# Kernel tuning notes

Measured on AMD Instinct MI355X. Metric: run time of the kernel, lower is better.

The kernel has to match this reference:

```python
import jax, jax.numpy as jnp
import numpy as np

DIM = 2048          # SDR dimension
CTX = 512           # top-down context (grid code) dimension
B = 8192            # batch of independent samples
N_PV = DIM // 4     # 512 PV interneurons
N_SV = DIM // 8     # 256 SOM/VIP interneurons
ALPHA_POS = 1.0 / 10.0   # dt / tau_pos
ALPHA_NEG = 1.0 / 10.0   # dt / tau_neg


def setup_inputs() -> dict:
    key = jax.random.key(0)
    ks = jax.random.split(key, 14)
    sc = 1.0 / np.sqrt(DIM)
    sc_sv = 1.0 / np.sqrt(N_SV)
    xav = np.sqrt(6.0 / (CTX + DIM))  # xavier uniform bound for predictor
    u = lambda k, shp, s: jax.random.uniform(k, shp, dtype=jnp.float32) * s
    return {
        "x_batch": jax.random.uniform(ks[0], (B, DIM), dtype=jnp.float32),
        "context_batch": jax.random.normal(ks[1], (B, CTX), dtype=jnp.float32),
        "r_pos_batch": jax.random.uniform(ks[2], (B, DIM), dtype=jnp.float32),
        "r_neg_batch": jax.random.uniform(ks[3], (B, DIM), dtype=jnp.float32),
        "W_pred": jax.random.uniform(ks[4], (DIM, CTX), jnp.float32, -xav, xav),
        "b_pred": jnp.zeros((DIM,), jnp.float32),
        "W_pv1_ff": u(ks[5], (N_PV, DIM), sc),
        "W_pv2_td": u(ks[6], (N_PV, DIM), sc),
        "W_vip_td": u(ks[7], (N_SV, DIM), sc),
        "W_som_in": u(ks[8], (N_SV, DIM), sc),
        "W_vip_som": u(ks[9], (N_SV, N_SV), sc_sv),
        "W_inh_pe_pos": u(ks[10], (DIM, N_PV), sc),
        "W_inh_pe_neg": u(ks[11], (DIM, N_PV), sc),
        "W_som_dend": u(ks[12], (DIM, N_SV), sc),
    }


def reference(x_batch, context_batch, r_pos_batch, r_neg_batch,
              W_pred, b_pred, W_pv1_ff, W_pv2_td, W_vip_td, W_som_in,
              W_vip_som, W_inh_pe_pos, W_inh_pe_neg, W_som_dend):
    relu = jax.nn.relu
    # top-down prediction: (B, CTX) @ (CTX, DIM) -> (B, DIM)
    predicted = context_batch @ W_pred.T + b_pred
    # interneuron circuit (Nemati 2025)
    r_pv1 = relu(x_batch @ W_pv1_ff.T)                               # (B, N_PV)
    r_pv2 = relu(predicted @ W_pv2_td.T)                             # (B, N_PV)
    r_vip = relu(predicted @ W_vip_td.T)                             # (B, N_SV)
    r_som = relu(relu(x_batch @ W_som_in.T) - r_vip @ W_vip_som.T)   # (B, N_SV)
    # signed prediction errors with somatic/dendritic inhibition
    pe_pos = relu(x_batch - predicted - r_pv2 @ W_inh_pe_pos.T)
    pe_neg = relu(predicted - x_batch - r_pv1 @ W_inh_pe_neg.T - r_som @ W_som_dend.T)
    # low-pass temporal filter of PE states
    new_r_pos = (1.0 - ALPHA_POS) * r_pos_batch + ALPHA_POS * pe_pos
    new_r_neg = (1.0 - ALPHA_NEG) * r_neg_batch + ALPHA_NEG * pe_neg
    return (new_r_pos, new_r_neg)
```

## Files before the change

kernel.cpp:

```cpp
#include <hip/hip_runtime.h>
#include <hip/hip_bf16.h>
#include <stdint.h>
#include <stddef.h>

#define DIMV 2048
#define CTXV 512
#define BV   8192
#define NPV  512
#define NSV  256

typedef __attribute__((ext_vector_type(8))) __bf16 bf16x8;
typedef __attribute__((ext_vector_type(4))) float f32x4;

enum { EPI_BIAS = 0, EPI_RELU = 1, EPI_SUBR = 2, EPI_FILT = 3 };

__device__ __forceinline__ void gload_lds16(const void* g, void* l) {
    __builtin_amdgcn_global_load_lds(
        (const __attribute__((address_space(1))) unsigned int*)g,
        (__attribute__((address_space(3))) unsigned int*)l,
        16, 0, 0);
}

struct CvtArgs {
    const float* src[11];
    __bf16*      dst[11];
};

__global__ __launch_bounds__(256) void cvt_all(CvtArgs a) {
    constexpr int NSEG = 11;
    constexpr unsigned cum[NSEG + 1] = {
        0u, 2097152u, 2621440u, 2752512u, 2883584u, 3014656u,
        3080192u, 3145728u, 3153920u, 3284992u, 3416064u, 3481600u};
    const unsigned total = cum[NSEG];
    for (unsigned c = blockIdx.x * blockDim.x + threadIdx.x; c < total;
         c += gridDim.x * blockDim.x) {
        const float* sp = a.src[0];
        __bf16*      dp = a.dst[0];
        unsigned     base = 0;
#pragma unroll
        for (int t = 1; t < NSEG; ++t) {
            const bool g = (c >= cum[t]);
            sp   = g ? a.src[t] : sp;
            dp   = g ? a.dst[t] : dp;
            base = g ? cum[t] : base;
        }
        const unsigned off = (c - base) * 8u;
        f32x4 v0 = *(const f32x4*)(sp + off);
        f32x4 v1 = *(const f32x4*)(sp + off + 4);
        bf16x8 o;
#pragma unroll
        for (int e = 0; e < 4; ++e) { o[e] = (__bf16)v0[e]; o[e + 4] = (__bf16)v1[e]; }
        *(bf16x8*)(dp + off) = o;
    }
}

template <int EPI>
__global__ __launch_bounds__(256)
void pe_gemm(const __bf16* __restrict__ A, int ldA,
             const __bf16* __restrict__ A2, int ldA2, int ksA,
             const __bf16* __restrict__ W1, int ldW1,
             const __bf16* __restrict__ W1k2, int ldW1k2, int ksW,
             const __bf16* __restrict__ W2, int ldW2,
             int NB1, int N1cols, int N2cols, int K, int nbx,
             const float* __restrict__ bias,
             const __bf16* __restrict__ subp,
             const __bf16* __restrict__ predb, const float* __restrict__ xf,
             float sgn, const float* __restrict__ rold,
             void* __restrict__ out1, void* __restrict__ out2)
{
    __shared__ __align__(16) __bf16 ldsA[128 * 32];
    __shared__ __align__(16) __bf16 ldsB[128 * 32];
    char* ldsAb = (char*)ldsA;
    char* ldsBb = (char*)ldsB;

    const int nwg = gridDim.x;
    const int bid = blockIdx.x;
    const int wg  = (bid & 7) * (nwg >> 3) + (bid >> 3);
    const int bx  = wg % nbx;
    const int by  = wg / nbx;
    const int m0  = bx * 128;
    const int n0  = by * 128;

    const bool reg2   = (W2 != nullptr) && (n0 >= NB1);
    const __bf16* Wa  = reg2 ? W2 : W1;
    const __bf16* Wb  = W1k2;
    const int wlda    = reg2 ? ldW2 : ldW1;
    const int wldb    = ldW1k2;
    const int kswcur  = reg2 ? K : ksW;
    const int nrow0   = reg2 ? (n0 - NB1) : n0;

    const int tid  = threadIdx.x;
    const int wave = tid >> 6;
    const int lane = tid & 63;
    const int lhi  = lane >> 4;
    const int llo  = lane & 15;
    const int wr   = wave >> 1;
    const int wc   = wave & 1;

    const f32x4 fzero = {0.f, 0.f, 0.f, 0.f};
    f32x4 acc[4][4];
#pragma unroll
    for (int i = 0; i < 4; ++i)
#pragma unroll
        for (int j = 0; j < 4; ++j) acc[i][j] = fzero;

    const int rins = lane >> 2;
    const int ch   = lane & 3;

    for (int k0 = 0; k0 < K; k0 += 32) {
        __syncthreads();
#pragma unroll
        for (int half = 0; half < 2; ++half) {
            const int rt = wave * 32 + half * 16 + rins;
            const int kc = ch ^ ((rt >> 1) & 3);
            const int kg = k0 + kc * 8;
            {
                const __bf16* src = (kg < ksA)
                    ? A  + (size_t)(m0 + rt) * ldA  + kg
                    : A2 + (size_t)(m0 + rt) * ldA2 + (kg - ksA);
                gload_lds16(src, ldsAb + wave * 2048 + half * 1024);
            }
            {
                const __bf16* src = (kg < kswcur)
                    ? Wa + (size_t)(nrow0 + rt) * wlda + kg
                    : Wb + (size_t)(nrow0 + rt) * wldb + (kg - kswcur);
                gload_lds16(src, ldsBb + wave * 2048 + half * 1024);
            }
        }
        __syncthreads();

        bf16x8 af[4], bfr[4];
#pragma unroll
        for (int i = 0; i < 4; ++i) {
            const int r  = wr * 64 + i * 16 + llo;
            const int pc = lhi ^ ((r >> 1) & 3);
            af[i] = *(const bf16x8*)(ldsAb + r * 64 + pc * 16);
        }
#pragma unroll
        for (int j = 0; j < 4; ++j) {
            const int r  = wc * 64 + j * 16 + llo;
            const int pc = lhi ^ ((r >> 1) & 3);
            bfr[j] = *(const bf16x8*)(ldsBb + r * 64 + pc * 16);
        }
#pragma unroll
        for (int i = 0; i < 4; ++i)
#pragma unroll
            for (int j = 0; j < 4; ++j)
                acc[i][j] = __builtin_amdgcn_mfma_f32_16x16x32_bf16(af[i], bfr[j], acc[i][j], 0, 0, 0);
    }

#pragma unroll
    for (int i = 0; i < 4; ++i) {
#pragma unroll
        for (int j = 0; j < 4; ++j) {
            const int colg = n0 + wc * 64 + j * 16 + llo;
#pragma unroll
            for (int r = 0; r < 4; ++r) {
                const int rowg = m0 + wr * 64 + i * 16 + lhi * 4 + r;
                float v = acc[i][j][r];
                if constexpr (EPI == EPI_BIAS) {
                    v += bias[colg];
                    ((__bf16*)out1)[(size_t)rowg * N1cols + colg] = (__bf16)v;
                } else if constexpr (EPI == EPI_RELU) {
                    v = fmaxf(v, 0.f);
                    if (colg < NB1)
                        ((__bf16*)out1)[(size_t)rowg * N1cols + colg] = (__bf16)v;
                    else
                        ((__bf16*)out2)[(size_t)rowg * N2cols + (colg - NB1)] = (__bf16)v;
                } else if constexpr (EPI == EPI_SUBR) {
                    const size_t idx = (size_t)rowg * N1cols + colg;
                    v = fmaxf((float)subp[idx] - v, 0.f);
                    ((__bf16*)out1)[idx] = (__bf16)v;
                } else {
                    const size_t idx = (size_t)rowg * 2048 + colg;
                    const float d = sgn * (xf[idx] - (float)predb[idx]) - v;
                    ((float*)out1)[idx] = 0.9f * rold[idx] + 0.1f * fmaxf(d, 0.f);
                }
            }
        }
    }
}

extern "C" void kernel_launch(void* const* d_in, const int* in_sizes, int n_in,
                              void* d_out, int out_size, void* d_ws, size_t ws_size,
                              hipStream_t stream) {
    (void)in_sizes; (void)n_in; (void)out_size; (void)ws_size;

    const float* x       = (const float*)d_in[0];
    const float* ctx     = (const float*)d_in[1];
    const float* r_pos   = (const float*)d_in[2];
    const float* r_neg   = (const float*)d_in[3];
    const float* Wpred   = (const float*)d_in[4];
    const float* bpred   = (const float*)d_in[5];
    const float* Wpv1    = (const float*)d_in[6];
    const float* Wpv2    = (const float*)d_in[7];
    const float* Wvip    = (const float*)d_in[8];
    const float* Wsomin  = (const float*)d_in[9];
    const float* Wvipsom = (const float*)d_in[10];
    const float* Wpepos  = (const float*)d_in[11];
    const float* Wpeneg  = (const float*)d_in[12];
    const float* Wsomd   = (const float*)d_in[13];

    char* ws = (char*)d_ws;
    __bf16* x_bf      = (__bf16*)ws; ws += (size_t)BV * DIMV * 2;
    __bf16* ctx_bf    = (__bf16*)ws; ws += (size_t)BV * CTXV * 2;
    __bf16* pred_bf   = (__bf16*)ws; ws += (size_t)BV * DIMV * 2;
    __bf16* rpv1_bf   = (__bf16*)ws; ws += (size_t)BV * NPV * 2;
    __bf16* rpv2_bf   = (__bf16*)ws; ws += (size_t)BV * NPV * 2;
    __bf16* rvip_bf   = (__bf16*)ws; ws += (size_t)BV * NSV * 2;
    __bf16* ssom_bf   = (__bf16*)ws; ws += (size_t)BV * NSV * 2;
    __bf16* rsom_bf   = (__bf16*)ws; ws += (size_t)BV * NSV * 2;
    __bf16* Wpred_bf  = (__bf16*)ws; ws += (size_t)DIMV * CTXV * 2;
    __bf16* Wpv1_bf   = (__bf16*)ws; ws += (size_t)NPV * DIMV * 2;
    __bf16* Wpv2_bf   = (__bf16*)ws; ws += (size_t)NPV * DIMV * 2;
    __bf16* Wvip_bf   = (__bf16*)ws; ws += (size_t)NSV * DIMV * 2;
    __bf16* Wsomin_bf = (__bf16*)ws; ws += (size_t)NSV * DIMV * 2;
    __bf16* Wvipsom_bf= (__bf16*)ws; ws += (size_t)NSV * NSV * 2;
    __bf16* Wpepos_bf = (__bf16*)ws; ws += (size_t)DIMV * NPV * 2;
    __bf16* Wpeneg_bf = (__bf16*)ws; ws += (size_t)DIMV * NPV * 2;
    __bf16* Wsomd_bf  = (__bf16*)ws; ws += (size_t)DIMV * NSV * 2;

    float* out_pos = (float*)d_out;
    float* out_neg = out_pos + (size_t)BV * DIMV;

    CvtArgs ca;
    ca.src[0] = x;       ca.dst[0] = x_bf;
    ca.src[1] = ctx;     ca.dst[1] = ctx_bf;
    ca.src[2] = Wpred;   ca.dst[2] = Wpred_bf;
    ca.src[3] = Wpv1;    ca.dst[3] = Wpv1_bf;
    ca.src[4] = Wpv2;    ca.dst[4] = Wpv2_bf;
    ca.src[5] = Wvip;    ca.dst[5] = Wvip_bf;
    ca.src[6] = Wsomin;  ca.dst[6] = Wsomin_bf;
    ca.src[7] = Wvipsom; ca.dst[7] = Wvipsom_bf;
    ca.src[8] = Wpepos;  ca.dst[8] = Wpepos_bf;
    ca.src[9] = Wpeneg;  ca.dst[9] = Wpeneg_bf;
    ca.src[10] = Wsomd;  ca.dst[10] = Wsomd_bf;
    cvt_all<<<dim3(2048), dim3(256), 0, stream>>>(ca);

    dim3 blk(256);

    pe_gemm<EPI_BIAS><<<dim3(1024), blk, 0, stream>>>(
        ctx_bf, CTXV, nullptr, 0, CTXV,
        Wpred_bf, CTXV, nullptr, 0, CTXV, nullptr, 0,
        DIMV, DIMV, 0, CTXV, 64,
        bpred, nullptr, nullptr, nullptr, 0.f, nullptr, pred_bf, nullptr);

    pe_gemm<EPI_RELU><<<dim3(384), blk, 0, stream>>>(
        x_bf, DIMV, nullptr, 0, DIMV,
        Wpv1_bf, DIMV, nullptr, 0, DIMV, Wsomin_bf, DIMV,
        NPV, NPV, NSV, DIMV, 64,
        nullptr, nullptr, nullptr, nullptr, 0.f, nullptr, rpv1_bf, ssom_bf);

    pe_gemm<EPI_RELU><<<dim3(384), blk, 0, stream>>>(
        pred_bf, DIMV, nullptr, 0, DIMV,
        Wpv2_bf, DIMV, nullptr, 0, DIMV, Wvip_bf, DIMV,
        NPV, NPV, NSV, DIMV, 64,
        nullptr, nullptr, nullptr, nullptr, 0.f, nullptr, rpv2_bf, rvip_bf);

    pe_gemm<EPI_SUBR><<<dim3(128), blk, 0, stream>>>(
        rvip_bf, NSV, nullptr, 0, NSV,
        Wvipsom_bf, NSV, nullptr, 0, NSV, nullptr, 0,
        NSV, NSV, 0, NSV, 64,
        nullptr, ssom_bf, nullptr, nullptr, 0.f, nullptr, rsom_bf, nullptr);

    pe_gemm<EPI_FILT><<<dim3(1024), blk, 0, stream>>>(
        rpv2_bf, NPV, nullptr, 0, NPV,
        Wpepos_bf, NPV, nullptr, 0, NPV, nullptr, 0,
        DIMV, DIMV, 0, NPV, 64,
        nullptr, nullptr, pred_bf, x, 1.f, r_pos, out_pos, nullptr);

    pe_gemm<EPI_FILT><<<dim3(1024), blk, 0, stream>>>(
        rpv1_bf, NPV, rsom_bf, NSV, NPV,
        Wpeneg_bf, NPV, Wsomd_bf, NSV, NPV, nullptr, 0,
        DIMV, DIMV, 0, NPV + NSV, 64,
        nullptr, nullptr, pred_bf, x, -1.f, r_neg, out_neg, nullptr);
}
```

Before: 353.9 us.

## Double-buffer GEMM LDS, merge independent GEMM launches, vectorize epilogues

Replaces the templated GEMM with a descriptor-driven kernel that runs two independent GEMMs in one launch (pred + pv1/som, and the pos/neg filter GEMMs), cutting launches from six to four and filling the device better. The K loop becomes double-buffered, so global-to-LDS loads for the next step overlap MFMA on the current one, with one barrier per step. Swapping the MFMA operands makes each lane hold four consecutive columns, which allows vectorized bf16x4/f32x4 epilogue stores. The filter epilogue now reads the bf16 copy of x instead of fp32 x, trading a little precision for less traffic. LDS use doubles and the epilogue type becomes a runtime branch.

```diff
diff --git a/kernel.cpp b/kernel.cpp
--- a/kernel.cpp
+++ b/kernel.cpp
@@ -10,9 +10,8 @@
 #define NSV  256
 
 typedef __attribute__((ext_vector_type(8))) __bf16 bf16x8;
+typedef __attribute__((ext_vector_type(4))) __bf16 bf16x4;
 typedef __attribute__((ext_vector_type(4))) float f32x4;
-
-enum { EPI_BIAS = 0, EPI_RELU = 1, EPI_SUBR = 2, EPI_FILT = 3 };
 
 __device__ __forceinline__ void gload_lds16(const void* g, void* l) {
     __builtin_amdgcn_global_load_lds(
@@ -54,40 +53,41 @@
     }
 }
 
-template <int EPI>
+struct GemmDesc {
+    const __bf16* A0; const __bf16* A1; int ldA0, ldA1;
+    const __bf16* W1; const __bf16* W2; const __bf16* W1b; int ldW, ldWb;
+    int ksplit;
+    int NB1;
+    int N1cols, N2cols;
+    int K;
+    int epi;
+    const float* bias;
+    const __bf16* subp;
+    const __bf16* xbf; const __bf16* predb; const float* rold; float sgn;
+    void* out1; void* out2;
+};
+
 __global__ __launch_bounds__(256)
-void pe_gemm(const __bf16* __restrict__ A, int ldA,
-             const __bf16* __restrict__ A2, int ldA2, int ksA,
-             const __bf16* __restrict__ W1, int ldW1,
-             const __bf16* __restrict__ W1k2, int ldW1k2, int ksW,
-             const __bf16* __restrict__ W2, int ldW2,
-             int NB1, int N1cols, int N2cols, int K, int nbx,
-             const float* __restrict__ bias,
-             const __bf16* __restrict__ subp,
-             const __bf16* __restrict__ predb, const float* __restrict__ xf,
-             float sgn, const float* __restrict__ rold,
-             void* __restrict__ out1, void* __restrict__ out2)
+void pe_gemm2(GemmDesc dA_, GemmDesc dB_, int splitWg)
 {
-    __shared__ __align__(16) __bf16 ldsA[128 * 32];
-    __shared__ __align__(16) __bf16 ldsB[128 * 32];
-    char* ldsAb = (char*)ldsA;
-    char* ldsBb = (char*)ldsB;
+    __shared__ __align__(16) char ldsA[2][8192];
+    __shared__ __align__(16) char ldsB[2][8192];
 
     const int nwg = gridDim.x;
     const int bid = blockIdx.x;
-    const int wg  = (bid & 7) * (nwg >> 3) + (bid >> 3);
-    const int bx  = wg % nbx;
-    const int by  = wg / nbx;
-    const int m0  = bx * 128;
-    const int n0  = by * 128;
-
-    const bool reg2   = (W2 != nullptr) && (n0 >= NB1);
-    const __bf16* Wa  = reg2 ? W2 : W1;
-    const __bf16* Wb  = W1k2;
-    const int wlda    = reg2 ? ldW2 : ldW1;
-    const int wldb    = ldW1k2;
-    const int kswcur  = reg2 ? K : ksW;
-    const int nrow0   = reg2 ? (n0 - NB1) : n0;
+    int wg = (bid & 7) * (nwg >> 3) + (bid >> 3);
+    const bool second = (wg >= splitWg);
+    if (second) wg -= splitWg;
+    const GemmDesc d = second ? dB_ : dA_;
+
+    const int bx = wg & 63;
+    const int by = wg >> 6;
+    const int m0 = bx * 128;
+    const int n0 = by * 128;
+
+    const bool reg2   = (n0 >= d.NB1);
+    const __bf16* Wk0 = reg2 ? d.W2 : d.W1;
+    const int n0r     = reg2 ? (n0 - d.NB1) : n0;
 
     const int tid  = threadIdx.x;
     const int wave = tid >> 6;
@@ -96,6 +96,8 @@
     const int llo  = lane & 15;
     const int wr   = wave >> 1;
     const int wc   = wave & 1;
+    const int rins = lane >> 2;
+    const int ch   = lane & 3;
 
     const f32x4 fzero = {0.f, 0.f, 0.f, 0.f};
     f32x4 acc[4][4];
@@ -104,78 +106,98 @@
 #pragma unroll
         for (int j = 0; j < 4; ++j) acc[i][j] = fzero;
 
-    const int rins = lane >> 2;
-    const int ch   = lane & 3;
-
-    for (int k0 = 0; k0 < K; k0 += 32) {
-        __syncthreads();
-#pragma unroll
-        for (int half = 0; half < 2; ++half) {
-            const int rt = wave * 32 + half * 16 + rins;
-            const int kc = ch ^ ((rt >> 1) & 3);
-            const int kg = k0 + kc * 8;
-            {
-                const __bf16* src = (kg < ksA)
-                    ? A  + (size_t)(m0 + rt) * ldA  + kg
-                    : A2 + (size_t)(m0 + rt) * ldA2 + (kg - ksA);
-                gload_lds16(src, ldsAb + wave * 2048 + half * 1024);
-            }
-            {
-                const __bf16* src = (kg < kswcur)
-                    ? Wa + (size_t)(nrow0 + rt) * wlda + kg
-                    : Wb + (size_t)(nrow0 + rt) * wldb + (kg - kswcur);
-                gload_lds16(src, ldsBb + wave * 2048 + half * 1024);
-            }
-        }
-        __syncthreads();
-
+    const int nsteps = d.K >> 5;
+
+#define STAGE2(S, BUF)                                                        \
+    {                                                                         \
+        const int k0_ = (S) * 32;                                             \
+        const bool sg1 = (k0_ >= d.ksplit);                                   \
+        const __bf16* As_ = sg1 ? d.A1  : d.A0;                               \
+        const __bf16* Ws_ = sg1 ? d.W1b : Wk0;                                \
+        const int la_ = sg1 ? d.ldA1 : d.ldA0;                                \
+        const int lw_ = sg1 ? d.ldWb : d.ldW;                                 \
+        const int kb_ = sg1 ? (k0_ - d.ksplit) : k0_;                         \
+        _Pragma("unroll")                                                     \
+        for (int half = 0; half < 2; ++half) {                                \
+            const int rt = wave * 32 + half * 16 + rins;                      \
+            const int kc = ch ^ ((rt >> 1) & 3);                              \
+            const int kk = kb_ + kc * 8;                                      \
+            gload_lds16(As_ + (size_t)(m0 + rt) * la_ + kk,                   \
+                        ldsA[BUF] + wave * 2048 + half * 1024);               \
+            gload_lds16(Ws_ + (size_t)(n0r + rt) * lw_ + kk,                  \
+                        ldsB[BUF] + wave * 2048 + half * 1024);               \
+        }                                                                     \
+    }
+
+    STAGE2(0, 0)
+    __syncthreads();
+    int cur = 0;
+    for (int s = 0; s < nsteps; ++s) {
+        if (s + 1 < nsteps) STAGE2(s + 1, cur ^ 1)
         bf16x8 af[4], bfr[4];
 #pragma unroll
         for (int i = 0; i < 4; ++i) {
             const int r  = wr * 64 + i * 16 + llo;
             const int pc = lhi ^ ((r >> 1) & 3);
-            af[i] = *(const bf16x8*)(ldsAb + r * 64 + pc * 16);
+            af[i] = *(const bf16x8*)(ldsA[cur] + r * 64 + pc * 16);
         }
 #pragma unroll
         for (int j = 0; j < 4; ++j) {
             const int r  = wc * 64 + j * 16 + llo;
             const int pc = lhi ^ ((r >> 1) & 3);
-            bfr[j] = *(const bf16x8*)(ldsBb + r * 64 + pc * 16);
+            bfr[j] = *(const bf16x8*)(ldsB[cur] + r * 64 + pc * 16);
         }
 #pragma unroll
         for (int i = 0; i < 4; ++i)
 #pragma unroll
             for (int j = 0; j < 4; ++j)
-                acc[i][j] = __builtin_amdgcn_mfma_f32_16x16x32_bf16(af[i], bfr[j], acc[i][j], 0, 0, 0);
+                acc[i][j] = __builtin_amdgcn_mfma_f32_16x16x32_bf16(bfr[j], af[i], acc[i][j], 0, 0, 0);
+        __syncthreads();
+        cur ^= 1;
     }
+#undef STAGE2
 
 #pragma unroll
     for (int i = 0; i < 4; ++i) {
 #pragma unroll
         for (int j = 0; j < 4; ++j) {
-            const int colg = n0 + wc * 64 + j * 16 + llo;
-#pragma unroll
-            for (int r = 0; r < 4; ++r) {
-                const int rowg = m0 + wr * 64 + i * 16 + lhi * 4 + r;
-                float v = acc[i][j][r];
-                if constexpr (EPI == EPI_BIAS) {
-                    v += bias[colg];
-                    ((__bf16*)out1)[(size_t)rowg * N1cols + colg] = (__bf16)v;
-                } else if constexpr (EPI == EPI_RELU) {
-                    v = fmaxf(v, 0.f);
-                    if (colg < NB1)
-                        ((__bf16*)out1)[(size_t)rowg * N1cols + colg] = (__bf16)v;
-                    else
-                        ((__bf16*)out2)[(size_t)rowg * N2cols + (colg - NB1)] = (__bf16)v;
-                } else if constexpr (EPI == EPI_SUBR) {
-                    const size_t idx = (size_t)rowg * N1cols + colg;
-                    v = fmaxf((float)subp[idx] - v, 0.f);
-                    ((__bf16*)out1)[idx] = (__bf16)v;
-                } else {
-                    const size_t idx = (size_t)rowg * 2048 + colg;
-                    const float d = sgn * (xf[idx] - (float)predb[idx]) - v;
-                    ((float*)out1)[idx] = 0.9f * rold[idx] + 0.1f * fmaxf(d, 0.f);
+            const int rowg = m0 + wr * 64 + i * 16 + llo;
+            const int colb = wc * 64 + j * 16 + lhi * 4;
+            if (d.epi == 0) {
+                const size_t idx = (size_t)rowg * d.N1cols + (n0 + colb);
+                f32x4 b4 = *(const f32x4*)(d.bias + n0 + colb);
+                bf16x4 o;
+#pragma unroll
+                for (int r = 0; r < 4; ++r) o[r] = (__bf16)(acc[i][j][r] + b4[r]);
+                *(bf16x4*)((__bf16*)d.out1 + idx) = o;
+            } else if (d.epi == 1) {
+                __bf16* op   = reg2 ? (__bf16*)d.out2 : (__bf16*)d.out1;
+                const int ldo = reg2 ? d.N2cols : d.N1cols;
+                const size_t idx = (size_t)rowg * ldo + (n0r + colb);
+                bf16x4 o;
+#pragma unroll
+                for (int r = 0; r < 4; ++r) o[r] = (__bf16)fmaxf(acc[i][j][r], 0.f);
+                *(bf16x4*)(op + idx) = o;
+            } else if (d.epi == 2) {
+                const size_t idx = (size_t)rowg * d.N1cols + (n0 + colb);
+                bf16x4 s4 = *(const bf16x4*)(d.subp + idx);
+                bf16x4 o;
+#pragma unroll
+                for (int r = 0; r < 4; ++r)
+                    o[r] = (__bf16)fmaxf((float)s4[r] - acc[i][j][r], 0.f);
+                *(bf16x4*)((__bf16*)d.out1 + idx) = o;
+            } else {
+                const size_t idx = (size_t)rowg * 2048 + (n0 + colb);
+                f32x4 rp  = *(const f32x4*)(d.rold + idx);
+                bf16x4 xb = *(const bf16x4*)(d.xbf + idx);
+                bf16x4 pb = *(const bf16x4*)(d.predb + idx);
+                f32x4 o;
+#pragma unroll
+                for (int r = 0; r < 4; ++r) {
+                    const float dd = d.sgn * ((float)xb[r] - (float)pb[r]);
+                    o[r] = 0.9f * rp[r] + 0.1f * fmaxf(dd - acc[i][j][r], 0.f);
                 }
+                *(f32x4*)((float*)d.out1 + idx) = o;
             }
         }
     }
@@ -237,41 +259,61 @@
     ca.src[10] = Wsomd;  ca.dst[10] = Wsomd_bf;
     cvt_all<<<dim3(2048), dim3(256), 0, stream>>>(ca);
 
-    dim3 blk(256);
-
-    pe_gemm<EPI_BIAS><<<dim3(1024), blk, 0, stream>>>(
-        ctx_bf, CTXV, nullptr, 0, CTXV,
-        Wpred_bf, CTXV, nullptr, 0, CTXV, nullptr, 0,
-        DIMV, DIMV, 0, CTXV, 64,
-        bpred, nullptr, nullptr, nullptr, 0.f, nullptr, pred_bf, nullptr);
-
-    pe_gemm<EPI_RELU><<<dim3(384), blk, 0, stream>>>(
-        x_bf, DIMV, nullptr, 0, DIMV,
-        Wpv1_bf, DIMV, nullptr, 0, DIMV, Wsomin_bf, DIMV,
-        NPV, NPV, NSV, DIMV, 64,
-        nullptr, nullptr, nullptr, nullptr, 0.f, nullptr, rpv1_bf, ssom_bf);
-
-    pe_gemm<EPI_RELU><<<dim3(384), blk, 0, stream>>>(
-        pred_bf, DIMV, nullptr, 0, DIMV,
-        Wpv2_bf, DIMV, nullptr, 0, DIMV, Wvip_bf, DIMV,
-        NPV, NPV, NSV, DIMV, 64,
-        nullptr, nullptr, nullptr, nullptr, 0.f, nullptr, rpv2_bf, rvip_bf);
-
-    pe_gemm<EPI_SUBR><<<dim3(128), blk, 0, stream>>>(
-        rvip_bf, NSV, nullptr, 0, NSV,
-        Wvipsom_bf, NSV, nullptr, 0, NSV, nullptr, 0,
-        NSV, NSV, 0, NSV, 64,
-        nullptr, ssom_bf, nullptr, nullptr, 0.f, nullptr, rsom_bf, nullptr);
-
-    pe_gemm<EPI_FILT><<<dim3(1024), blk, 0, stream>>>(
-        rpv2_bf, NPV, nullptr, 0, NPV,
-        Wpepos_bf, NPV, nullptr, 0, NPV, nullptr, 0,
-        DIMV, DIMV, 0, NPV, 64,
-        nullptr, nullptr, pred_bf, x, 1.f, r_pos, out_pos, nullptr);
-
-    pe_gemm<EPI_FILT><<<dim3(1024), blk, 0, stream>>>(
-        rpv1_bf, NPV, rsom_bf, NSV, NPV,
-        Wpeneg_bf, NPV, Wsomd_bf, NSV, NPV, nullptr, 0,
-        DIMV, DIMV, 0, NPV + NSV, 64,
-        nullptr, nullptr, pred_bf, x, -1.f, r_neg, out_neg, nullptr);
+    const int BIG = 1 << 28;
+    GemmDesc dz;
+    dz.A0 = dz.A1 = nullptr; dz.ldA0 = dz.ldA1 = 0;
+    dz.W1 = dz.W2 = dz.W1b = nullptr; dz.ldW = dz.ldWb = 0;
+    dz.ksplit = BIG; dz.NB1 = BIG; dz.N1cols = dz.N2cols = 0; dz.K = 32;
+    dz.epi = 1; dz.bias = nullptr; dz.subp = nullptr;
+    dz.xbf = dz.predb = nullptr; dz.rold = nullptr; dz.sgn = 1.f;
+    dz.out1 = dz.out2 = nullptr;
+
+    GemmDesc d_pred = dz;
+    d_pred.A0 = ctx_bf; d_pred.A1 = ctx_bf; d_pred.ldA0 = d_pred.ldA1 = CTXV;
+    d_pred.W1 = d_pred.W2 = d_pred.W1b = Wpred_bf; d_pred.ldW = d_pred.ldWb = CTXV;
+    d_pred.K = CTXV; d_pred.N1cols = DIMV; d_pred.epi = 0;
+    d_pred.bias = bpred; d_pred.out1 = pred_bf;
+
+    GemmDesc d_23 = dz;
+    d_23.A0 = d_23.A1 = x_bf; d_23.ldA0 = d_23.ldA1 = DIMV;
+    d_23.W1 = Wpv1_bf; d_23.W2 = Wsomin_bf; d_23.W1b = Wpv1_bf;
+    d_23.ldW = d_23.ldWb = DIMV;
+    d_23.K = DIMV; d_23.NB1 = NPV; d_23.N1cols = NPV; d_23.N2cols = NSV;
+    d_23.epi = 1; d_23.out1 = rpv1_bf; d_23.out2 = ssom_bf;
+
+    pe_gemm2<<<dim3(1408), dim3(256), 0, stream>>>(d_pred, d_23, 1024);
+
+    GemmDesc d_45 = dz;
+    d_45.A0 = d_45.A1 = pred_bf; d_45.ldA0 = d_45.ldA1 = DIMV;
+    d_45.W1 = Wpv2_bf; d_45.W2 = Wvip_bf; d_45.W1b = Wpv2_bf;
+    d_45.ldW = d_45.ldWb = DIMV;
+    d_45.K = DIMV; d_45.NB1 = NPV; d_45.N1cols = NPV; d_45.N2cols = NSV;
+    d_45.epi = 1; d_45.out1 = rpv2_bf; d_45.out2 = rvip_bf;
+
+    pe_gemm2<<<dim3(384), dim3(256), 0, stream>>>(d_45, d_45, 384);
+
+    GemmDesc d_som = dz;
+    d_som.A0 = d_som.A1 = rvip_bf; d_som.ldA0 = d_som.ldA1 = NSV;
+    d_som.W1 = d_som.W2 = d_som.W1b = Wvipsom_bf; d_som.ldW = d_som.ldWb = NSV;
+    d_som.K = NSV; d_som.N1cols = NSV; d_som.epi = 2;
+    d_som.subp = ssom_bf; d_som.out1 = rsom_bf;
+
+    pe_gemm2<<<dim3(128), dim3(256), 0, stream>>>(d_som, d_som, 128);
+
+    GemmDesc d_f7 = dz;
+    d_f7.A0 = d_f7.A1 = rpv2_bf; d_f7.ldA0 = d_f7.ldA1 = NPV;
+    d_f7.W1 = d_f7.W2 = d_f7.W1b = Wpepos_bf; d_f7.ldW = d_f7.ldWb = NPV;
+    d_f7.K = NPV; d_f7.N1cols = DIMV; d_f7.epi = 3;
+    d_f7.xbf = x_bf; d_f7.predb = pred_bf; d_f7.rold = r_pos; d_f7.sgn = 1.f;
+    d_f7.out1 = out_pos;
+
+    GemmDesc d_f8 = dz;
+    d_f8.A0 = rpv1_bf; d_f8.A1 = rsom_bf; d_f8.ldA0 = NPV; d_f8.ldA1 = NSV;
+    d_f8.W1 = d_f8.W2 = Wpeneg_bf; d_f8.W1b = Wsomd_bf;
+    d_f8.ldW = NPV; d_f8.ldWb = NSV; d_f8.ksplit = NPV;
+    d_f8.K = NPV + NSV; d_f8.N1cols = DIMV; d_f8.epi = 3;
+    d_f8.xbf = x_bf; d_f8.predb = pred_bf; d_f8.rold = r_neg; d_f8.sgn = -1.f;
+    d_f8.out1 = out_neg;
+
+    pe_gemm2<<<dim3(2048), dim3(256), 0, stream>>>(d_f7, d_f8, 1024);
 }
```

New measurement: 379.8 us. +7.3%, slower.
